# Optimization experiments

Hardware: AMD Instinct MI355X
Metric: run time of the kernel (lower is better)

The kernel has to match this reference:

```python
import jax, jax.numpy as jnp
import numpy as np

B, V, C, NB, KS, OUT = 2, 20000, 32, 12, 9, 32


def setup_inputs() -> dict:
    key = jax.random.key(0)
    k1, k2, k3, k4 = jax.random.split(key, 4)
    x = jax.random.normal(k1, (B, V, C), jnp.float32)
    # padded neighbor table: index 0 == padding row, valid indices 1..V
    adj = jax.random.randint(k2, (V, NB), 0, V + 1, dtype=jnp.int32)
    # GlorotNormal-ish scales
    W = jax.random.normal(k3, (C, KS, OUT), jnp.float32) * np.float32(np.sqrt(2.0 / (C + KS * OUT)))
    u = jax.random.normal(k4, (C, KS), jnp.float32) * np.float32(np.sqrt(2.0 / (C + KS)))
    c = jnp.zeros((KS,), jnp.float32)
    b = jnp.zeros((OUT,), jnp.float32)
    return {"x": x, "W": W, "u": u, "c": c, "b": b, "adj": adj}


def reference(x, W, u, c, b, adj):
    Bb, Vv, Cc = x.shape
    ks, out = W.shape[1], W.shape[2]
    # inverse neighbor count (0 index means padding); 0 where no neighbors
    deg = jnp.count_nonzero(adj, axis=-1).astype(x.dtype)            # [V]
    inv_deg = jnp.where(deg > 0, 1.0 / deg, jnp.zeros_like(deg))     # [V]

    # wx = x @ reshape(W) -> per-vertex kernelized features
    wx = jnp.einsum('bvc,cko->bvko', x, W)                           # [B,V,ks,out]
    wx_pad = jnp.concatenate([jnp.zeros((Bb, 1, ks, out), x.dtype), wx], axis=1)
    nb_wx = wx_pad[:, adj]                                           # [B,V,nb,ks,out]

    # attention logits: u(x_i) - u(x_j) + c, softmax over kernel axis
    ux = jnp.einsum('bvc,ck->bvk', x, u)                             # [B,V,ks]
    ux_pad = jnp.concatenate([jnp.zeros((Bb, 1, ks), x.dtype), ux], axis=1)
    nb_ux = ux_pad[:, adj]                                           # [B,V,nb,ks]
    q = jax.nn.softmax(ux[:, :, None, :] - nb_ux + c, axis=-1)       # [B,V,nb,ks]

    # softmax-weighted sum over neighbors, then mean (via inv_deg) over kernels
    agg = jnp.einsum('bvnk,bvnko->bvko', q, nb_wx)                   # [B,V,ks,out]
    res = jnp.einsum('bvko,v->bvo', agg, inv_deg) + b                # [B,V,out]
    return jax.nn.relu(res)
```

## Files before the change

kernel.cpp:

```cpp
#include <hip/hip_runtime.h>
#include <math.h>

#define PBDIM 256
#define BDIM  64

constexpr int Vc = 20000, Cc = 32, NBc = 12, KSc = 9, OUTc = 32;
constexpr int NTASK = 40000;
constexpr int UXP   = 12;
constexpr int MT    = 16;
constexpr int NITER = NTASK / MT;
constexpr int WFE   = KSc * 2 * 64 * 8;

typedef __attribute__((ext_vector_type(8))) short short8;
typedef __attribute__((ext_vector_type(4))) float floatx4;

__global__ __launch_bounds__(PBDIM)
void prep_kernel(const float* __restrict__ x, const float* __restrict__ u,
                 const float* __restrict__ W, float* __restrict__ ux,
                 unsigned short* __restrict__ wf)
{
    if (blockIdx.x < 157) {
        __shared__ float us[Cc * KSc];
        for (int i = threadIdx.x; i < Cc * KSc; i += PBDIM) us[i] = u[i];
        __syncthreads();
        const int row = blockIdx.x * PBDIM + threadIdx.x;
        if (row >= NTASK) return;
        const float4* xr = (const float4*)(x + row * Cc);
        float4 xv[8];
#pragma unroll
        for (int i = 0; i < 8; ++i) xv[i] = xr[i];
        float acc[KSc];
#pragma unroll
        for (int k = 0; k < KSc; ++k) acc[k] = 0.f;
#pragma unroll
        for (int c = 0; c < Cc; ++c) {
            const float xc = ((const float*)xv)[c];
#pragma unroll
            for (int k = 0; k < KSc; ++k) acc[k] = fmaf(xc, us[c * KSc + k], acc[k]);
        }
        float4* o4 = (float4*)(ux + row * UXP);
        o4[0] = make_float4(acc[0], acc[1], acc[2], acc[3]);
        o4[1] = make_float4(acc[4], acc[5], acc[6], acc[7]);
        o4[2] = make_float4(acc[8], 0.f, 0.f, 0.f);
    } else {
        const int e = (blockIdx.x - 157) * PBDIM + threadIdx.x;
        if (e >= WFE) return;
        const int j = e & 7;
        const int l = (e >> 3) & 63;
        const int h = (e >> 9) & 1;
        const int k = e >> 10;
        const int c = (l >> 4) * 8 + j;
        const int o = (l & 15) + 16 * h;
        const float w = W[(c * KSc + k) * OUTc + o];
        const unsigned int bits = __float_as_uint(w);
        const unsigned short hi = (unsigned short)(bits >> 16);
        const float hif = __uint_as_float(bits & 0xFFFF0000u);
        const float lof = w - hif;
        const unsigned short lo = (unsigned short)(__float_as_uint(lof) >> 16);
        wf[e]       = hi;
        wf[WFE + e] = lo;
    }
}

__global__ __launch_bounds__(BDIM, 3)
void fused_kernel(const float* __restrict__ x, const float* __restrict__ cvec,
                  const float* __restrict__ bvec, const int* __restrict__ adj,
                  const float* __restrict__ ux, const unsigned short* __restrict__ wf,
                  float* __restrict__ out)
{
    __shared__ __align__(16) float qs[MT][KSc][NBc];

    const int l64 = threadIdx.x;
    const int oo  = l64 & 15;
    const int cb  = l64 >> 4;
    const int t0  = blockIdx.x * MT;

    float ck[KSc];
#pragma unroll
    for (int k = 0; k < KSc; ++k) ck[k] = cvec[k];

    int   tP[3], nP[3], rowP[3];
    bool  predP[3];
    float uo[3][12], un[3][12];
#pragma unroll
    for (int p = 0; p < 3; ++p) {
        const int unit = p * 64 + l64;
        const int t    = (unit * 171) >> 11;
        const int n    = unit - t * 12;
        const int task = t0 + t;
        const int bb   = (task >= Vc) ? 1 : 0;
        const int v    = task - bb * Vc;
        const int jn   = adj[v * NBc + n];
        predP[p] = (jn != 0);
        rowP[p]  = predP[p] ? (bb * Vc + jn - 1) : 0;
        tP[p] = t; nP[p] = n;
    }
#pragma unroll
    for (int p = 0; p < 3; ++p) {
        const float4* uo4 = (const float4*)(ux + (t0 + tP[p]) * UXP);
        const float4* un4 = (const float4*)(ux + rowP[p] * UXP);
        *(float4*)&uo[p][0] = uo4[0]; *(float4*)&uo[p][4] = uo4[1]; *(float4*)&uo[p][8] = uo4[2];
        *(float4*)&un[p][0] = un4[0]; *(float4*)&un[p][4] = un4[1]; *(float4*)&un[p][8] = un4[2];
    }
#pragma unroll
    for (int p = 0; p < 3; ++p) {
        float e[KSc];
        float mx = -3.0e38f;
#pragma unroll
        for (int k = 0; k < KSc; ++k) {
            e[k] = uo[p][k] - un[p][k] + ck[k];
            mx = fmaxf(mx, e[k]);
        }
        float s = 0.f;
#pragma unroll
        for (int k = 0; k < KSc; ++k) { e[k] = __expf(e[k] - mx); s += e[k]; }
        const float r = predP[p] ? (1.f / s) : 0.f;
#pragma unroll
        for (int k = 0; k < KSc; ++k) qs[tP[p]][k][nP[p]] = e[k] * r;
    }

    const int tA   = l64 & 15;
    const int task = t0 + tA;
    const int bb   = (task >= Vc) ? 1 : 0;
    const int v    = task - bb * Vc;
    int rows[NBc];
    float inv_local;
    {
        const int4* ar = (const int4*)(adj + v * NBc);
        const int4 a0 = ar[0], a1 = ar[1], a2 = ar[2];
        int jv[NBc];
        jv[0] = a0.x; jv[1] = a0.y; jv[2]  = a0.z; jv[3]  = a0.w;
        jv[4] = a1.x; jv[5] = a1.y; jv[6]  = a1.z; jv[7]  = a1.w;
        jv[8] = a2.x; jv[9] = a2.y; jv[10] = a2.z; jv[11] = a2.w;
        int d = 0;
#pragma unroll
        for (int n = 0; n < NBc; ++n) {
            const bool pr = (jv[n] != 0);
            d += pr ? 1 : 0;
            rows[n] = pr ? (bb * Vc + jv[n] - 1) : 0;
        }
        inv_local = (d > 0) ? 1.f / (float)d : 0.f;
    }

    float y[KSc][8];
#pragma unroll
    for (int k = 0; k < KSc; ++k)
#pragma unroll
        for (int j = 0; j < 8; ++j) y[k][j] = 0.f;

#pragma unroll
    for (int nb = 0; nb < 3; ++nb) {
        float xs[4][8];
#pragma unroll
        for (int i = 0; i < 4; ++i) {
            const float4* xp = (const float4*)(x + rows[nb * 4 + i] * Cc + cb * 8);
            *(float4*)&xs[i][0] = xp[0];
            *(float4*)&xs[i][4] = xp[1];
        }
#pragma unroll
        for (int k = 0; k < KSc; ++k) {
            const float4 q4 = *(const float4*)&qs[tA][k][nb * 4];
#pragma unroll
            for (int j = 0; j < 8; ++j) {
                float a = y[k][j];
                a = fmaf(q4.x, xs[0][j], a);
                a = fmaf(q4.y, xs[1][j], a);
                a = fmaf(q4.z, xs[2][j], a);
                a = fmaf(q4.w, xs[3][j], a);
                y[k][j] = a;
            }
        }
    }

    floatx4 acc0 = {0.f, 0.f, 0.f, 0.f};
    floatx4 acc1 = {0.f, 0.f, 0.f, 0.f};
#pragma unroll
    for (int k = 0; k < KSc; ++k) {
        short8 ah, al;
#pragma unroll
        for (int j = 0; j < 8; ++j) {
            const unsigned int yb = __float_as_uint(y[k][j]);
            ah[j] = (short)(yb >> 16);
            const float hif = __uint_as_float(yb & 0xFFFF0000u);
            const float lof = y[k][j] - hif;
            al[j] = (short)(__float_as_uint(lof) >> 16);
        }
        const short8 bh0 = *(const short8*)(wf + ((k * 2 + 0) * 64 + l64) * 8);
        const short8 bh1 = *(const short8*)(wf + ((k * 2 + 1) * 64 + l64) * 8);
        const short8 bl0 = *(const short8*)(wf + WFE + ((k * 2 + 0) * 64 + l64) * 8);
        const short8 bl1 = *(const short8*)(wf + WFE + ((k * 2 + 1) * 64 + l64) * 8);
        acc0 = __builtin_amdgcn_mfma_f32_16x16x32_bf16(ah, bh0, acc0, 0, 0, 0);
        acc0 = __builtin_amdgcn_mfma_f32_16x16x32_bf16(al, bh0, acc0, 0, 0, 0);
        acc0 = __builtin_amdgcn_mfma_f32_16x16x32_bf16(ah, bl0, acc0, 0, 0, 0);
        acc1 = __builtin_amdgcn_mfma_f32_16x16x32_bf16(ah, bh1, acc1, 0, 0, 0);
        acc1 = __builtin_amdgcn_mfma_f32_16x16x32_bf16(al, bh1, acc1, 0, 0, 0);
        acc1 = __builtin_amdgcn_mfma_f32_16x16x32_bf16(ah, bl1, acc1, 0, 0, 0);
    }

    const float b0 = bvec[oo], b1 = bvec[oo + 16];
#pragma unroll
    for (int r = 0; r < 4; ++r) {
        const int tl   = cb * 4 + r;
        const float nv = __shfl(inv_local, tl, 64);
        const int tsk  = t0 + tl;
        out[tsk * OUTc + oo]      = fmaxf(fmaf(acc0[r], nv, b0), 0.f);
        out[tsk * OUTc + oo + 16] = fmaxf(fmaf(acc1[r], nv, b1), 0.f);
    }
}

extern "C" void kernel_launch(void* const* d_in, const int* in_sizes, int n_in,
                              void* d_out, int out_size, void* d_ws, size_t ws_size,
                              hipStream_t stream)
{
    const float* x    = (const float*)d_in[0];
    const float* W    = (const float*)d_in[1];
    const float* u    = (const float*)d_in[2];
    const float* cvec = (const float*)d_in[3];
    const float* bvec = (const float*)d_in[4];
    const int*   adj  = (const int*)d_in[5];
    float* out = (float*)d_out;

    float*          ux = (float*)d_ws;
    unsigned short* wf = (unsigned short*)((char*)d_ws + 1920000);

    prep_kernel<<<157 + 36, PBDIM, 0, stream>>>(x, u, W, ux, wf);
    fused_kernel<<<NITER, BDIM, 0, stream>>>(x, cvec, bvec, adj, ux, wf, out);
}
```

Baseline: 88.07 us.

## Store x and ux in fp16 and switch split MFMA to f16

The prep kernel now writes fp16 copies of x and of the ux attention logits, and the fused kernel gathers those half-width rows in place of the fp32 originals, halving gather bytes. The split-precision MFMA path changes from bf16 hi/lo to f16 hi/lo. The neighbor x gathers are also issued up front, before the softmax computation, to overlap latency. The cost is an extra fp16 x write in prep and reduced precision for x and ux, which are rounded to fp16 with no low-part correction.

```diff
diff --git a/kernel.cpp b/kernel.cpp
--- a/kernel.cpp
+++ b/kernel.cpp
@@ -6,18 +6,19 @@
 
 constexpr int Vc = 20000, Cc = 32, NBc = 12, KSc = 9, OUTc = 32;
 constexpr int NTASK = 40000;
-constexpr int UXP   = 12;
 constexpr int MT    = 16;
 constexpr int NITER = NTASK / MT;
+constexpr int UXH   = 16;
+constexpr int XHS   = 32;
 constexpr int WFE   = KSc * 2 * 64 * 8;
 
-typedef __attribute__((ext_vector_type(8))) short short8;
+typedef _Float16 half8 __attribute__((ext_vector_type(8)));
 typedef __attribute__((ext_vector_type(4))) float floatx4;
 
 __global__ __launch_bounds__(PBDIM)
 void prep_kernel(const float* __restrict__ x, const float* __restrict__ u,
-                 const float* __restrict__ W, float* __restrict__ ux,
-                 unsigned short* __restrict__ wf)
+                 const float* __restrict__ W, _Float16* __restrict__ uxh,
+                 _Float16* __restrict__ xh, _Float16* __restrict__ wf)
 {
     if (blockIdx.x < 157) {
         __shared__ float us[Cc * KSc];
@@ -38,10 +39,18 @@
 #pragma unroll
             for (int k = 0; k < KSc; ++k) acc[k] = fmaf(xc, us[c * KSc + k], acc[k]);
         }
-        float4* o4 = (float4*)(ux + row * UXP);
-        o4[0] = make_float4(acc[0], acc[1], acc[2], acc[3]);
-        o4[1] = make_float4(acc[4], acc[5], acc[6], acc[7]);
-        o4[2] = make_float4(acc[8], 0.f, 0.f, 0.f);
+        half8 o;
+#pragma unroll
+        for (int k = 0; k < 8; ++k) o[k] = (_Float16)acc[k];
+        *(half8*)(uxh + row * UXH) = o;
+        uxh[row * UXH + 8] = (_Float16)acc[8];
+#pragma unroll
+        for (int q = 0; q < 4; ++q) {
+            half8 hx;
+#pragma unroll
+            for (int j = 0; j < 8; ++j) hx[j] = (_Float16)((const float*)xv)[q * 8 + j];
+            *(half8*)(xh + row * XHS + q * 8) = hx;
+        }
     } else {
         const int e = (blockIdx.x - 157) * PBDIM + threadIdx.x;
         if (e >= WFE) return;
@@ -52,20 +61,17 @@
         const int c = (l >> 4) * 8 + j;
         const int o = (l & 15) + 16 * h;
         const float w = W[(c * KSc + k) * OUTc + o];
-        const unsigned int bits = __float_as_uint(w);
-        const unsigned short hi = (unsigned short)(bits >> 16);
-        const float hif = __uint_as_float(bits & 0xFFFF0000u);
-        const float lof = w - hif;
-        const unsigned short lo = (unsigned short)(__float_as_uint(lof) >> 16);
-        wf[e]       = hi;
-        wf[WFE + e] = lo;
+        const _Float16 wh = (_Float16)w;
+        const _Float16 wl = (_Float16)(w - (float)wh);
+        wf[e]       = wh;
+        wf[WFE + e] = wl;
     }
 }
 
 __global__ __launch_bounds__(BDIM, 3)
-void fused_kernel(const float* __restrict__ x, const float* __restrict__ cvec,
-                  const float* __restrict__ bvec, const int* __restrict__ adj,
-                  const float* __restrict__ ux, const unsigned short* __restrict__ wf,
+void fused_kernel(const float* __restrict__ cvec, const float* __restrict__ bvec,
+                  const int* __restrict__ adj, const _Float16* __restrict__ uxh,
+                  const _Float16* __restrict__ xh, const _Float16* __restrict__ wf,
                   float* __restrict__ out)
 {
     __shared__ __align__(16) float qs[MT][KSc][NBc];
@@ -78,46 +84,6 @@
     float ck[KSc];
 #pragma unroll
     for (int k = 0; k < KSc; ++k) ck[k] = cvec[k];
-
-    int   tP[3], nP[3], rowP[3];
-    bool  predP[3];
-    float uo[3][12], un[3][12];
-#pragma unroll
-    for (int p = 0; p < 3; ++p) {
-        const int unit = p * 64 + l64;
-        const int t    = (unit * 171) >> 11;
-        const int n    = unit - t * 12;
-        const int task = t0 + t;
-        const int bb   = (task >= Vc) ? 1 : 0;
-        const int v    = task - bb * Vc;
-        const int jn   = adj[v * NBc + n];
-        predP[p] = (jn != 0);
-        rowP[p]  = predP[p] ? (bb * Vc + jn - 1) : 0;
-        tP[p] = t; nP[p] = n;
-    }
-#pragma unroll
-    for (int p = 0; p < 3; ++p) {
-        const float4* uo4 = (const float4*)(ux + (t0 + tP[p]) * UXP);
-        const float4* un4 = (const float4*)(ux + rowP[p] * UXP);
-        *(float4*)&uo[p][0] = uo4[0]; *(float4*)&uo[p][4] = uo4[1]; *(float4*)&uo[p][8] = uo4[2];
-        *(float4*)&un[p][0] = un4[0]; *(float4*)&un[p][4] = un4[1]; *(float4*)&un[p][8] = un4[2];
-    }
-#pragma unroll
-    for (int p = 0; p < 3; ++p) {
-        float e[KSc];
-        float mx = -3.0e38f;
-#pragma unroll
-        for (int k = 0; k < KSc; ++k) {
-            e[k] = uo[p][k] - un[p][k] + ck[k];
-            mx = fmaxf(mx, e[k]);
-        }
-        float s = 0.f;
-#pragma unroll
-        for (int k = 0; k < KSc; ++k) { e[k] = __expf(e[k] - mx); s += e[k]; }
-        const float r = predP[p] ? (1.f / s) : 0.f;
-#pragma unroll
-        for (int k = 0; k < KSc; ++k) qs[tP[p]][k][nP[p]] = e[k] * r;
-    }
 
     const int tA   = l64 & 15;
     const int task = t0 + tA;
@@ -141,6 +107,42 @@
         }
         inv_local = (d > 0) ? 1.f / (float)d : 0.f;
     }
+    half8 xr[NBc];
+#pragma unroll
+    for (int n = 0; n < NBc; ++n)
+        xr[n] = *(const half8*)(xh + rows[n] * XHS + cb * 8);
+
+#pragma unroll
+    for (int p = 0; p < 3; ++p) {
+        const int unit = p * 64 + l64;
+        const int t    = (unit * 171) >> 11;
+        const int n    = unit - t * 12;
+        const int tk   = t0 + t;
+        const int bbp  = (tk >= Vc) ? 1 : 0;
+        const int vp   = tk - bbp * Vc;
+        const int jn   = adj[vp * NBc + n];
+        const bool pred = (jn != 0);
+        const int row = pred ? (bbp * Vc + jn - 1) : 0;
+        const half8 uo8 = *(const half8*)(uxh + tk * UXH);
+        const _Float16 uoe = uxh[tk * UXH + 8];
+        const half8 un8 = *(const half8*)(uxh + row * UXH);
+        const _Float16 une = uxh[row * UXH + 8];
+        float e[KSc];
+        float mx = -3.0e38f;
+#pragma unroll
+        for (int k = 0; k < 8; ++k) {
+            e[k] = (float)uo8[k] - (float)un8[k] + ck[k];
+            mx = fmaxf(mx, e[k]);
+        }
+        e[8] = (float)uoe - (float)une + ck[8];
+        mx = fmaxf(mx, e[8]);
+        float s = 0.f;
+#pragma unroll
+        for (int k = 0; k < KSc; ++k) { e[k] = __expf(e[k] - mx); s += e[k]; }
+        const float r = pred ? (1.f / s) : 0.f;
+#pragma unroll
+        for (int k = 0; k < KSc; ++k) qs[t][k][n] = e[k] * r;
+    }
 
     float y[KSc][8];
 #pragma unroll
@@ -152,11 +154,9 @@
     for (int nb = 0; nb < 3; ++nb) {
         float xs[4][8];
 #pragma unroll
-        for (int i = 0; i < 4; ++i) {
-            const float4* xp = (const float4*)(x + rows[nb * 4 + i] * Cc + cb * 8);
-            *(float4*)&xs[i][0] = xp[0];
-            *(float4*)&xs[i][4] = xp[1];
-        }
+        for (int i = 0; i < 4; ++i)
+#pragma unroll
+            for (int j = 0; j < 8; ++j) xs[i][j] = (float)xr[nb * 4 + i][j];
 #pragma unroll
         for (int k = 0; k < KSc; ++k) {
             const float4 q4 = *(const float4*)&qs[tA][k][nb * 4];
@@ -176,25 +176,24 @@
     floatx4 acc1 = {0.f, 0.f, 0.f, 0.f};
 #pragma unroll
     for (int k = 0; k < KSc; ++k) {
-        short8 ah, al;
+        half8 ah, al;
 #pragma unroll
         for (int j = 0; j < 8; ++j) {
-            const unsigned int yb = __float_as_uint(y[k][j]);
-            ah[j] = (short)(yb >> 16);
-            const float hif = __uint_as_float(yb & 0xFFFF0000u);
-            const float lof = y[k][j] - hif;
-            al[j] = (short)(__float_as_uint(lof) >> 16);
-        }
-        const short8 bh0 = *(const short8*)(wf + ((k * 2 + 0) * 64 + l64) * 8);
-        const short8 bh1 = *(const short8*)(wf + ((k * 2 + 1) * 64 + l64) * 8);
-        const short8 bl0 = *(const short8*)(wf + WFE + ((k * 2 + 0) * 64 + l64) * 8);
-        const short8 bl1 = *(const short8*)(wf + WFE + ((k * 2 + 1) * 64 + l64) * 8);
-        acc0 = __builtin_amdgcn_mfma_f32_16x16x32_bf16(ah, bh0, acc0, 0, 0, 0);
-        acc0 = __builtin_amdgcn_mfma_f32_16x16x32_bf16(al, bh0, acc0, 0, 0, 0);
-        acc0 = __builtin_amdgcn_mfma_f32_16x16x32_bf16(ah, bl0, acc0, 0, 0, 0);
-        acc1 = __builtin_amdgcn_mfma_f32_16x16x32_bf16(ah, bh1, acc1, 0, 0, 0);
-        acc1 = __builtin_amdgcn_mfma_f32_16x16x32_bf16(al, bh1, acc1, 0, 0, 0);
-        acc1 = __builtin_amdgcn_mfma_f32_16x16x32_bf16(ah, bl1, acc1, 0, 0, 0);
+            const float yy = y[k][j];
+            const _Float16 hh = (_Float16)yy;
+            ah[j] = hh;
+            al[j] = (_Float16)(yy - (float)hh);
+        }
+        const half8 bh0 = *(const half8*)(wf + ((k * 2 + 0) * 64 + l64) * 8);
+        const half8 bh1 = *(const half8*)(wf + ((k * 2 + 1) * 64 + l64) * 8);
+        const half8 bl0 = *(const half8*)(wf + WFE + ((k * 2 + 0) * 64 + l64) * 8);
+        const half8 bl1 = *(const half8*)(wf + WFE + ((k * 2 + 1) * 64 + l64) * 8);
+        acc0 = __builtin_amdgcn_mfma_f32_16x16x32_f16(ah, bh0, acc0, 0, 0, 0);
+        acc0 = __builtin_amdgcn_mfma_f32_16x16x32_f16(al, bh0, acc0, 0, 0, 0);
+        acc0 = __builtin_amdgcn_mfma_f32_16x16x32_f16(ah, bl0, acc0, 0, 0, 0);
+        acc1 = __builtin_amdgcn_mfma_f32_16x16x32_f16(ah, bh1, acc1, 0, 0, 0);
+        acc1 = __builtin_amdgcn_mfma_f32_16x16x32_f16(al, bh1, acc1, 0, 0, 0);
+        acc1 = __builtin_amdgcn_mfma_f32_16x16x32_f16(ah, bl1, acc1, 0, 0, 0);
     }
 
     const float b0 = bvec[oo], b1 = bvec[oo + 16];
@@ -220,9 +219,10 @@
     const int*   adj  = (const int*)d_in[5];
     float* out = (float*)d_out;
 
-    float*          ux = (float*)d_ws;
-    unsigned short* wf = (unsigned short*)((char*)d_ws + 1920000);
-
-    prep_kernel<<<157 + 36, PBDIM, 0, stream>>>(x, u, W, ux, wf);
-    fused_kernel<<<NITER, BDIM, 0, stream>>>(x, cvec, bvec, adj, ux, wf, out);
+    _Float16* uxh = (_Float16*)d_ws;
+    _Float16* xh  = (_Float16*)((char*)d_ws + 1280000);
+    _Float16* wf  = (_Float16*)((char*)d_ws + 1280000 + 2560000);
+
+    prep_kernel<<<157 + 36, PBDIM, 0, stream>>>(x, u, W, uxh, xh, wf);
+    fused_kernel<<<NITER, BDIM, 0, stream>>>(cvec, bvec, adj, uxh, xh, wf, out);
 }
```

After: 87.75 us. About the same (-0.4%).
